# Kernel optimization log

Hardware: AMD Instinct MI355X
Metric: run time of the kernel (lower is better)

The kernel has to match this reference:

```python
import jax, jax.numpy as jnp
import numpy as np

N_M, N_D, E = 20000, 8000, 200000
F_IN, H, O = 384, 512, 256  # feature dim, hidden_channels, out_channels
H1 = O * 2                  # conv1 output channels = 512


def setup_inputs() -> dict:
    key = jax.random.key(0)
    ks = jax.random.split(key, 32)

    def w(k, shape):
        return jax.random.normal(k, shape, dtype=jnp.float32) * 0.02

    inp = {
        # node features
        "mirna_feat": jax.random.normal(ks[0], (N_M, F_IN), dtype=jnp.float32),
        "dis_feat": jax.random.normal(ks[1], (N_D, F_IN), dtype=jnp.float32),
        # node ids and edge list (miRNA -> disease); reverse edges are the flip
        "mirna_node_id": jnp.arange(N_M, dtype=jnp.int32),
        "dis_node_id": jnp.arange(N_D, dtype=jnp.int32),
        "edge_src": jax.random.randint(ks[2], (E,), 0, N_M, dtype=jnp.int32),
        "edge_dst": jax.random.randint(ks[3], (E,), 0, N_D, dtype=jnp.int32),
        # input projections + embeddings
        "Wm": w(ks[4], (F_IN, H)), "bm": jnp.zeros((H,), jnp.float32),
        "Wd": w(ks[5], (F_IN, H)), "bd": jnp.zeros((H,), jnp.float32),
        "mirna_emb": w(ks[6], (N_M, H)),
        "dis_emb": w(ks[7], (N_D, H)),
        # layer1 SAGEConv per edge type (md: miRNA->disease, dm: reverse)
        "W1_md_l": w(ks[8], (H, H1)), "b1_md": jnp.zeros((H1,), jnp.float32), "W1_md_r": w(ks[9], (H, H1)),
        "W1_dm_l": w(ks[10], (H, H1)), "b1_dm": jnp.zeros((H1,), jnp.float32), "W1_dm_r": w(ks[11], (H, H1)),
        # layer2 SAGEConv per edge type
        "W2_md_l": w(ks[12], (H1, O)), "b2_md": jnp.zeros((O,), jnp.float32), "W2_md_r": w(ks[13], (H1, O)),
        "W2_dm_l": w(ks[14], (H1, O)), "b2_dm": jnp.zeros((O,), jnp.float32), "W2_dm_r": w(ks[15], (H1, O)),
    }
    return inp


def _mean_agg(x_src, src_idx, dst_idx, n_dst):
    # gather src features per edge, segment-mean onto destinations (0 for isolated nodes)
    msg = jnp.take(x_src, src_idx, axis=0)               # [E, d]
    agg = jax.ops.segment_sum(msg, dst_idx, num_segments=n_dst)
    cnt = jax.ops.segment_sum(jnp.ones((dst_idx.shape[0],), x_src.dtype), dst_idx, num_segments=n_dst)
    return agg / jnp.maximum(cnt, 1.0)[:, None]


def _sage(x_src, x_dst, src_idx, dst_idx, Wl, bl, Wr):
    mean = _mean_agg(x_src, src_idx, dst_idx, x_dst.shape[0])
    return mean @ Wl + bl + x_dst @ Wr


def reference(mirna_feat, dis_feat, mirna_node_id, dis_node_id, edge_src, edge_dst,
              Wm, bm, Wd, bd, mirna_emb, dis_emb,
              W1_md_l, b1_md, W1_md_r, W1_dm_l, b1_dm, W1_dm_r,
              W2_md_l, b2_md, W2_md_r, W2_dm_l, b2_dm, W2_dm_r):
    # input encoders
    x_m = mirna_feat @ Wm + bm + jnp.take(mirna_emb, mirna_node_id, axis=0)
    x_d = dis_feat @ Wd + bd + jnp.take(dis_emb, dis_node_id, axis=0)
    # hetero SAGE layer 1 (each dst type has exactly one incoming edge type)
    h_d = _sage(x_m, x_d, edge_src, edge_dst, W1_md_l, b1_md, W1_md_r)
    h_m = _sage(x_d, x_m, edge_dst, edge_src, W1_dm_l, b1_dm, W1_dm_r)
    h_m, h_d = jax.nn.relu(h_m), jax.nn.relu(h_d)
    # hetero SAGE layer 2
    o_d = _sage(h_m, h_d, edge_src, edge_dst, W2_md_l, b2_md, W2_md_r)
    o_m = _sage(h_d, h_m, edge_dst, edge_src, W2_dm_l, b2_dm, W2_dm_r)
    return (o_m, o_d)
```

## Files before the change

### kernel.cpp

```cpp
#include <hip/hip_runtime.h>

#define DEVI __device__ __forceinline__

typedef __attribute__((ext_vector_type(8))) short bf16x8;
typedef __attribute__((ext_vector_type(4))) float f32x4;

static constexpr int NM = 20000, ND = 8000, NE = 200000;
static constexpr int FIN = 384, H = 512, H1 = 512, O = 256;

DEVI float bf2f(unsigned int u){ union{unsigned int i; float f;}v; v.i=u<<16; return v.f; }
DEVI unsigned int f2bf(float f){ union{float f; unsigned int i;}v; v.f=f;
  return (v.i + 0x7FFFu + ((v.i>>16)&1u))>>16; }

DEVI void gload16(const void* g, void* l){
  __builtin_amdgcn_global_load_lds((const __attribute__((address_space(1))) unsigned int*)g,
                                   (__attribute__((address_space(3))) unsigned int*)l, 16, 0, 0);
}

struct GPart {
  const unsigned short* A0;
  const unsigned short* A1;
  const unsigned short* WT;
  const float* bias;
  const float* emb;
  const int* ids;
  void* out;
  int M;
  int nbx;
};

template<int EPI>
__global__ __launch_bounds__(512, 8)
void gemm8w(GPart P0, GPart P1, int KA, int Ktot, int N)
{
  __shared__ unsigned short sA[2][128*32];
  __shared__ unsigned short sB[2][128*32];

  int bx = blockIdx.x;
  const bool snd = (bx >= P0.nbx);
  if (snd) bx -= P0.nbx;
  const unsigned short* A0  = snd ? P1.A0  : P0.A0;
  const unsigned short* A1  = snd ? P1.A1  : P0.A1;
  const unsigned short* WT  = snd ? P1.WT  : P0.WT;
  const float* bias         = snd ? P1.bias: P0.bias;
  const float* emb          = snd ? P1.emb : P0.emb;
  const int*   ids          = snd ? P1.ids : P0.ids;
  void*        outp         = snd ? P1.out : P0.out;
  const int    M            = snd ? P1.M   : P0.M;

  const int tid  = threadIdx.x;
  const int lane = tid & 63;
  const int wv   = tid >> 6;
  const int wr   = wv >> 1;
  const int wc   = wv & 1;
  const int bm0  = bx * 128;
  const int bn0  = blockIdx.y * 128;

  f32x4 acc[2][4];
  #pragma unroll
  for (int m=0;m<2;++m)
    #pragma unroll
    for (int n=0;n<4;++n) acc[m][n] = (f32x4){0.f,0.f,0.f,0.f};

  const int r = tid >> 2;
  const int c = tid & 3;
  const int KT = Ktot >> 5;

  auto STAGE = [&](int buf, int kt){
    const int kbase = kt << 5;
    const unsigned short* Ap; int ka, astr;
    if (kbase < KA) { Ap = A0; ka = kbase;      astr = KA; }
    else            { Ap = A1; ka = kbase - KA; astr = Ktot - KA; }
    int grA = bm0 + r; grA = grA < M ? grA : M-1;
    const int cc = (c ^ ((r>>1) & 3)) * 8;
    gload16(Ap + (size_t)grA*astr       + ka    + cc, &sA[buf][r*32 + c*8]);
    gload16(WT + (size_t)(bn0+r)*Ktot   + kbase + cc, &sB[buf][r*32 + c*8]);
  };

  STAGE(0, 0);
  __syncthreads();
  int cur = 0;
  for (int kt = 0; kt < KT; ++kt) {
    if (kt + 1 < KT) STAGE(cur ^ 1, kt + 1);
    bf16x8 af[2], bfr[4];
    #pragma unroll
    for (int m=0;m<2;++m){
      const int rl = wr*32 + m*16 + (lane&15);
      const int ch = (lane>>4) ^ ((rl>>1) & 3);
      af[m] = *(const bf16x8*)&sA[cur][rl*32 + ch*8];
    }
    #pragma unroll
    for (int n=0;n<4;++n){
      const int rl = wc*64 + n*16 + (lane&15);
      const int ch = (lane>>4) ^ ((rl>>1) & 3);
      bfr[n] = *(const bf16x8*)&sB[cur][rl*32 + ch*8];
    }
    #pragma unroll
    for (int m=0;m<2;++m)
      #pragma unroll
      for (int n=0;n<4;++n)
        acc[m][n] = __builtin_amdgcn_mfma_f32_16x16x32_bf16(af[m], bfr[n], acc[m][n], 0,0,0);
    __syncthreads();
    cur ^= 1;
  }

  const int cl = lane & 15;
  const int rg = lane >> 4;
  #pragma unroll
  for (int n=0;n<4;++n){
    const int col = bn0 + wc*64 + n*16 + cl;
    const float bv = bias[col];
    #pragma unroll
    for (int m=0;m<2;++m){
      const int rowb = bm0 + wr*32 + m*16 + rg*4;
      #pragma unroll
      for (int j=0;j<4;++j){
        const int row = rowb + j;
        if (row < M) {
          float v = acc[m][n][j] + bv;
          if constexpr (EPI==0) v += emb[(size_t)ids[row]*N + col];
          if constexpr (EPI==1) v = v > 0.f ? v : 0.f;
          if constexpr (EPI==2) ((float*)outp)[(size_t)row*N + col] = v;
          else ((unsigned short*)outp)[(size_t)row*N + col] = (unsigned short)f2bf(v);
        }
      }
    }
  }
}

__global__ __launch_bounds__(256)
void agg2(const unsigned short* __restrict__ Xm, const unsigned short* __restrict__ Xd,
          const int* __restrict__ offm, const int* __restrict__ ebs,
          const int* __restrict__ offd, const int* __restrict__ ebd,
          unsigned short* __restrict__ aggm, unsigned short* __restrict__ aggd)
{
  int node = blockIdx.x*4 + (threadIdx.x>>6);
  const unsigned short* X; const int* off; const int* nbr; unsigned short* out;
  if (node < NM){ X = Xd; off = offm; nbr = ebs; out = aggm; }
  else          { node -= NM; X = Xm; off = offd; nbr = ebd; out = aggd; }
  const int lane = threadIdx.x & 63;
  const int s = off[node], e = off[node+1];
  float a[8] = {0.f,0.f,0.f,0.f,0.f,0.f,0.f,0.f};
  for (int j = s; j < e; ++j){
    const int src = nbr[j];
    const uint4 v = *(const uint4*)(X + (size_t)src*H + lane*8);
    a[0]+=bf2f(v.x&0xffffu); a[1]+=bf2f(v.x>>16);
    a[2]+=bf2f(v.y&0xffffu); a[3]+=bf2f(v.y>>16);
    a[4]+=bf2f(v.z&0xffffu); a[5]+=bf2f(v.z>>16);
    a[6]+=bf2f(v.w&0xffffu); a[7]+=bf2f(v.w>>16);
  }
  const float inv = (e > s) ? 1.0f/(float)(e - s) : 0.0f;
  uint4 o;
  o.x = f2bf(a[0]*inv) | (f2bf(a[1]*inv)<<16);
  o.y = f2bf(a[2]*inv) | (f2bf(a[3]*inv)<<16);
  o.z = f2bf(a[4]*inv) | (f2bf(a[5]*inv)<<16);
  o.w = f2bf(a[6]*inv) | (f2bf(a[7]*inv)<<16);
  *(uint4*)(out + (size_t)node*H + lane*8) = o;
}

DEVI void tpart(int t, const float* __restrict__ in, unsigned short* __restrict__ out,
                int K, int N, int koff, int Kt)
{
  const int n = t / K, k = t - n*K;
  out[(size_t)n*Kt + koff + k] = (unsigned short)f2bf(in[(size_t)k*N + n]);
}

static constexpr int PREPW_BLOCKS = 7680;
static constexpr int CVT_BLOCKS   = 10500;
static constexpr int HIST_BLOCKS  = (NE + 255)/256;

__global__ __launch_bounds__(256)
void prep_all(const float* Wm, const float* Wd,
              const float* W1mdl, const float* W1mdr, const float* W1dml, const float* W1dmr,
              const float* W2mdl, const float* W2mdr, const float* W2dml, const float* W2dmr,
              unsigned short* WmT, unsigned short* WdT,
              unsigned short* W1mdT, unsigned short* W1dmT,
              unsigned short* W2mdT, unsigned short* W2dmT,
              const float* fm, const float* fd, unsigned short* om, unsigned short* od,
              const int* esrc, const int* edst, int* degm, int* degd)
{
  const int b = blockIdx.x;
  if (b < PREPW_BLOCKS) {
    int t = b*256 + threadIdx.x;
    const int sE = FIN*H, s1 = H*H1, s2 = H1*O;
    if (t < sE){ tpart(t, Wm,    WmT,   FIN, H, 0,   FIN ); return; } t -= sE;
    if (t < sE){ tpart(t, Wd,    WdT,   FIN, H, 0,   FIN ); return; } t -= sE;
    if (t < s1){ tpart(t, W1mdl, W1mdT, H,  H1, 0,   1024); return; } t -= s1;
    if (t < s1){ tpart(t, W1mdr, W1mdT, H,  H1, 512, 1024); return; } t -= s1;
    if (t < s1){ tpart(t, W1dml, W1dmT, H,  H1, 0,   1024); return; } t -= s1;
    if (t < s1){ tpart(t, W1dmr, W1dmT, H,  H1, 512, 1024); return; } t -= s1;
    if (t < s2){ tpart(t, W2mdl, W2mdT, H1, O,  0,   1024); return; } t -= s2;
    if (t < s2){ tpart(t, W2mdr, W2mdT, H1, O,  512, 1024); return; } t -= s2;
    if (t < s2){ tpart(t, W2dml, W2dmT, H1, O,  0,   1024); return; } t -= s2;
    if (t < s2){ tpart(t, W2dmr, W2dmT, H1, O,  512, 1024); return; }
  } else if (b < PREPW_BLOCKS + CVT_BLOCKS) {
    const long nm = (long)NM*FIN/4, nd = (long)ND*FIN/4;
    const long i = (long)(b - PREPW_BLOCKS)*256 + threadIdx.x;
    if (i >= nm+nd) return;
    const float4 v = (i < nm) ? ((const float4*)fm)[i] : ((const float4*)fd)[i-nm];
    uint2 o; o.x = f2bf(v.x) | (f2bf(v.y)<<16); o.y = f2bf(v.z) | (f2bf(v.w)<<16);
    if (i < nm) ((uint2*)om)[i] = o; else ((uint2*)od)[i-nm] = o;
  } else {
    const int e = (b - PREPW_BLOCKS - CVT_BLOCKS)*256 + threadIdx.x;
    if (e < NE){ atomicAdd(&degd[edst[e]], 1); atomicAdd(&degm[esrc[e]], 1); }
  }
}

__global__ __launch_bounds__(256)
void scan_k(const int* __restrict__ degd, int* __restrict__ offd, int* __restrict__ curd,
            const int* __restrict__ degm, int* __restrict__ offm, int* __restrict__ curm)
{
  const int* deg; int* off; int* cur; int n;
  if (blockIdx.x == 0){ deg=degd; off=offd; cur=curd; n=ND; }
  else                { deg=degm; off=offm; cur=curm; n=NM; }
  __shared__ int ps[257];
  const int t = threadIdx.x;
  const int chunk = (n + 255) >> 8;
  int lo = t*chunk;     if (lo > n) lo = n;
  int hi = lo + chunk;  if (hi > n) hi = n;
  int s = 0;
  for (int i=lo;i<hi;++i) s += deg[i];
  ps[t+1] = s;
  if (t==0) ps[0] = 0;
  __syncthreads();
  if (t==0){ for (int i=1;i<=256;++i) ps[i] += ps[i-1]; }
  __syncthreads();
  int run = ps[t];
  for (int i=lo;i<hi;++i){ off[i]=run; cur[i]=run; run += deg[i]; }
  if (t==0) off[n] = ps[256];
}

__global__ __launch_bounds__(256)
void fill_k(const int* __restrict__ esrc, const int* __restrict__ edst,
            int* __restrict__ curd, int* __restrict__ curm,
            int* __restrict__ ebd, int* __restrict__ ebs)
{
  const int e = blockIdx.x*256 + threadIdx.x;
  if (e < NE){
    const int s = esrc[e], d = edst[e];
    ebd[atomicAdd(&curd[d],1)] = s;
    ebs[atomicAdd(&curm[s],1)] = d;
  }
}

extern "C" void kernel_launch(void* const* d_in, const int* in_sizes, int n_in,
                              void* d_out, int out_size, void* d_ws, size_t ws_size,
                              hipStream_t stream)
{
  (void)in_sizes; (void)n_in; (void)out_size; (void)ws_size;
  const float* mirna_feat=(const float*)d_in[0];
  const float* dis_feat  =(const float*)d_in[1];
  const int*   m_id =(const int*)d_in[2];
  const int*   d_id =(const int*)d_in[3];
  const int*   esrc =(const int*)d_in[4];
  const int*   edst =(const int*)d_in[5];
  const float* Wm=(const float*)d_in[6];  const float* bm=(const float*)d_in[7];
  const float* Wd=(const float*)d_in[8];  const float* bd=(const float*)d_in[9];
  const float* m_emb=(const float*)d_in[10]; const float* d_emb=(const float*)d_in[11];
  const float* W1mdl=(const float*)d_in[12]; const float* b1md=(const float*)d_in[13];
  const float* W1mdr=(const float*)d_in[14];
  const float* W1dml=(const float*)d_in[15]; const float* b1dm=(const float*)d_in[16];
  const float* W1dmr=(const float*)d_in[17];
  const float* W2mdl=(const float*)d_in[18]; const float* b2md=(const float*)d_in[19];
  const float* W2mdr=(const float*)d_in[20];
  const float* W2dml=(const float*)d_in[21]; const float* b2dm=(const float*)d_in[22];
  const float* W2dmr=(const float*)d_in[23];

  size_t off = 0;
  char* base = (char*)d_ws;
  auto alloc = [&](size_t bytes)->void*{
    off = (off + 255) & ~(size_t)255;
    void* p = base + off; off += bytes; return p;
  };
  unsigned short* featm = (unsigned short*)alloc((size_t)NM*FIN*2);
  unsigned short* featd = (unsigned short*)alloc((size_t)ND*FIN*2);
  unsigned short* WmT   = (unsigned short*)alloc((size_t)H*FIN*2);
  unsigned short* WdT   = (unsigned short*)alloc((size_t)H*FIN*2);
  unsigned short* W1mdT = (unsigned short*)alloc((size_t)H1*1024*2);
  unsigned short* W1dmT = (unsigned short*)alloc((size_t)H1*1024*2);
  unsigned short* W2mdT = (unsigned short*)alloc((size_t)O*1024*2);
  unsigned short* W2dmT = (unsigned short*)alloc((size_t)O*1024*2);
  unsigned short* xm    = (unsigned short*)alloc((size_t)NM*H*2);
  unsigned short* xd    = (unsigned short*)alloc((size_t)ND*H*2);
  unsigned short* aggm  = (unsigned short*)alloc((size_t)NM*H*2);
  unsigned short* aggd  = (unsigned short*)alloc((size_t)ND*H*2);
  unsigned short* hm    = (unsigned short*)alloc((size_t)NM*H1*2);
  unsigned short* hd    = (unsigned short*)alloc((size_t)ND*H1*2);
  int* degd = (int*)alloc((size_t)(ND+NM)*4);
  int* degm = degd + ND;
  int* offd = (int*)alloc((size_t)(ND+1)*4);
  int* offm = (int*)alloc((size_t)(NM+1)*4);
  int* curd = (int*)alloc((size_t)ND*4);
  int* curm = (int*)alloc((size_t)NM*4);
  int* ebd  = (int*)alloc((size_t)NE*4);
  int* ebs  = (int*)alloc((size_t)NE*4);

  hipMemsetAsync(degd, 0, (size_t)(ND+NM)*4, stream);
  prep_all<<<PREPW_BLOCKS + CVT_BLOCKS + HIST_BLOCKS, 256, 0, stream>>>(
      Wm,Wd,W1mdl,W1mdr,W1dml,W1dmr,W2mdl,W2mdr,W2dml,W2dmr,
      WmT,WdT,W1mdT,W1dmT,W2mdT,W2dmT,
      mirna_feat, dis_feat, featm, featd,
      esrc, edst, degm, degd);
  scan_k<<<2,256,0,stream>>>(degd, offd, curd, degm, offm, curm);
  fill_k<<<(NE+255)/256,256,0,stream>>>(esrc, edst, curd, curm, ebd, ebs);

  {
    GPart p0{featm, featm, WmT, bm, m_emb, m_id, xm, NM, 157};
    GPart p1{featd, featd, WdT, bd, d_emb, d_id, xd, ND, 63};
    gemm8w<0><<<dim3(220,4),512,0,stream>>>(p0, p1, FIN, FIN, H);
  }
  agg2<<<(NM+ND)/4,256,0,stream>>>(xm, xd, offm, ebs, offd, ebd, aggm, aggd);
  {
    GPart p0{aggm, xm, W1dmT, b1dm, nullptr, nullptr, hm, NM, 157};
    GPart p1{aggd, xd, W1mdT, b1md, nullptr, nullptr, hd, ND, 63};
    gemm8w<1><<<dim3(220,4),512,0,stream>>>(p0, p1, H, 1024, H1);
  }
  agg2<<<(NM+ND)/4,256,0,stream>>>(hm, hd, offm, ebs, offd, ebd, aggm, aggd);
  float* out_m = (float*)d_out;
  float* out_d = out_m + (size_t)NM*O;
  {
    GPart p0{aggm, hm, W2dmT, b2dm, nullptr, nullptr, out_m, NM, 157};
    GPart p1{aggd, hd, W2mdT, b2md, nullptr, nullptr, out_d, ND, 63};
    gemm8w<2><<<dim3(220,2),512,0,stream>>>(p0, p1, H1, 1024, O);
  }
}
```

Before: 527.5 us.

## Triple-buffer GEMM LDS pipeline and pre-convert embeddings to bf16

The GEMM kernel moves from double to triple buffering of LDS tiles. It prefetches three k-steps ahead, waits with explicit vmcnt/lgkmcnt counters and raw barriers, and lowers the occupancy hint to 6 waves, all to hide global-load latency better. Separately, the embedding tables are converted to bf16 in the prep kernel, written into the hm/hd buffers before those are used, so the encoder epilogue reads half the bytes. The cost is an extra conversion pass over the embeddings and more LDS per block. The clamped redundant prefetch on the last tiles also adds some extra loads.

```diff
diff --git a/kernel.cpp b/kernel.cpp
--- a/kernel.cpp
+++ b/kernel.cpp
@@ -22,7 +22,7 @@
   const unsigned short* A1;
   const unsigned short* WT;
   const float* bias;
-  const float* emb;
+  const unsigned short* emb;
   const int* ids;
   void* out;
   int M;
@@ -30,11 +30,11 @@
 };
 
 template<int EPI>
-__global__ __launch_bounds__(512, 8)
+__global__ __launch_bounds__(512, 6)
 void gemm8w(GPart P0, GPart P1, int KA, int Ktot, int N)
 {
-  __shared__ unsigned short sA[2][128*32];
-  __shared__ unsigned short sB[2][128*32];
+  __shared__ unsigned short sA[3][128*32];
+  __shared__ unsigned short sB[3][128*32];
 
   int bx = blockIdx.x;
   const bool snd = (bx >= P0.nbx);
@@ -43,7 +43,7 @@
   const unsigned short* A1  = snd ? P1.A1  : P0.A1;
   const unsigned short* WT  = snd ? P1.WT  : P0.WT;
   const float* bias         = snd ? P1.bias: P0.bias;
-  const float* emb          = snd ? P1.emb : P0.emb;
+  const unsigned short* emb = snd ? P1.emb : P0.emb;
   const int*   ids          = snd ? P1.ids : P0.ids;
   void*        outp         = snd ? P1.out : P0.out;
   const int    M            = snd ? P1.M   : P0.M;
@@ -77,11 +77,11 @@
     gload16(WT + (size_t)(bn0+r)*Ktot   + kbase + cc, &sB[buf][r*32 + c*8]);
   };
 
-  STAGE(0, 0);
-  __syncthreads();
+  STAGE(0, 0); STAGE(1, 1); STAGE(2, 2);
   int cur = 0;
   for (int kt = 0; kt < KT; ++kt) {
-    if (kt + 1 < KT) STAGE(cur ^ 1, kt + 1);
+    asm volatile("s_waitcnt vmcnt(4)" ::: "memory");
+    __builtin_amdgcn_s_barrier();
     bf16x8 af[2], bfr[4];
     #pragma unroll
     for (int m=0;m<2;++m){
@@ -100,8 +100,12 @@
       #pragma unroll
       for (int n=0;n<4;++n)
         acc[m][n] = __builtin_amdgcn_mfma_f32_16x16x32_bf16(af[m], bfr[n], acc[m][n], 0,0,0);
-    __syncthreads();
-    cur ^= 1;
+    asm volatile("s_waitcnt lgkmcnt(0)" ::: "memory");
+    __builtin_amdgcn_sched_barrier(0);
+    __builtin_amdgcn_s_barrier();
+    const int nxt = (kt+3 < KT) ? (kt+3) : (KT-1);
+    STAGE(cur, nxt);
+    cur = (cur==2) ? 0 : cur+1;
   }
 
   const int cl = lane & 15;
@@ -118,7 +122,7 @@
         const int row = rowb + j;
         if (row < M) {
           float v = acc[m][n][j] + bv;
-          if constexpr (EPI==0) v += emb[(size_t)ids[row]*N + col];
+          if constexpr (EPI==0) v += bf2f(emb[(size_t)ids[row]*N + col]);
           if constexpr (EPI==1) v = v > 0.f ? v : 0.f;
           if constexpr (EPI==2) ((float*)outp)[(size_t)row*N + col] = v;
           else ((unsigned short*)outp)[(size_t)row*N + col] = (unsigned short)f2bf(v);
@@ -167,6 +171,7 @@
 
 static constexpr int PREPW_BLOCKS = 7680;
 static constexpr int CVT_BLOCKS   = 10500;
+static constexpr int EMB_BLOCKS   = 14000;
 static constexpr int HIST_BLOCKS  = (NE + 255)/256;
 
 __global__ __launch_bounds__(256)
@@ -177,6 +182,7 @@
               unsigned short* W1mdT, unsigned short* W1dmT,
               unsigned short* W2mdT, unsigned short* W2dmT,
               const float* fm, const float* fd, unsigned short* om, unsigned short* od,
+              const float* memb, const float* demb, unsigned short* embm, unsigned short* embd,
               const int* esrc, const int* edst, int* degm, int* degd)
 {
   const int b = blockIdx.x;
@@ -200,8 +206,15 @@
     const float4 v = (i < nm) ? ((const float4*)fm)[i] : ((const float4*)fd)[i-nm];
     uint2 o; o.x = f2bf(v.x) | (f2bf(v.y)<<16); o.y = f2bf(v.z) | (f2bf(v.w)<<16);
     if (i < nm) ((uint2*)om)[i] = o; else ((uint2*)od)[i-nm] = o;
+  } else if (b < PREPW_BLOCKS + CVT_BLOCKS + EMB_BLOCKS) {
+    const long nm = (long)NM*H/4, nd = (long)ND*H/4;
+    const long i = (long)(b - PREPW_BLOCKS - CVT_BLOCKS)*256 + threadIdx.x;
+    if (i >= nm+nd) return;
+    const float4 v = (i < nm) ? ((const float4*)memb)[i] : ((const float4*)demb)[i-nm];
+    uint2 o; o.x = f2bf(v.x) | (f2bf(v.y)<<16); o.y = f2bf(v.z) | (f2bf(v.w)<<16);
+    if (i < nm) ((uint2*)embm)[i] = o; else ((uint2*)embd)[i-nm] = o;
   } else {
-    const int e = (b - PREPW_BLOCKS - CVT_BLOCKS)*256 + threadIdx.x;
+    const int e = (b - PREPW_BLOCKS - CVT_BLOCKS - EMB_BLOCKS)*256 + threadIdx.x;
     if (e < NE){ atomicAdd(&degd[edst[e]], 1); atomicAdd(&degm[esrc[e]], 1); }
   }
 }
@@ -295,18 +308,22 @@
   int* ebd  = (int*)alloc((size_t)NE*4);
   int* ebs  = (int*)alloc((size_t)NE*4);
 
+  unsigned short* embm = hm;
+  unsigned short* embd = hd;
+
   hipMemsetAsync(degd, 0, (size_t)(ND+NM)*4, stream);
-  prep_all<<<PREPW_BLOCKS + CVT_BLOCKS + HIST_BLOCKS, 256, 0, stream>>>(
+  prep_all<<<PREPW_BLOCKS + CVT_BLOCKS + EMB_BLOCKS + HIST_BLOCKS, 256, 0, stream>>>(
       Wm,Wd,W1mdl,W1mdr,W1dml,W1dmr,W2mdl,W2mdr,W2dml,W2dmr,
       WmT,WdT,W1mdT,W1dmT,W2mdT,W2dmT,
       mirna_feat, dis_feat, featm, featd,
+      m_emb, d_emb, embm, embd,
       esrc, edst, degm, degd);
   scan_k<<<2,256,0,stream>>>(degd, offd, curd, degm, offm, curm);
   fill_k<<<(NE+255)/256,256,0,stream>>>(esrc, edst, curd, curm, ebd, ebs);
 
   {
-    GPart p0{featm, featm, WmT, bm, m_emb, m_id, xm, NM, 157};
-    GPart p1{featd, featd, WdT, bd, d_emb, d_id, xd, ND, 63};
+    GPart p0{featm, featm, WmT, bm, embm, m_id, xm, NM, 157};
+    GPart p1{featd, featd, WdT, bd, embd, d_id, xd, ND, 63};
     gemm8w<0><<<dim3(220,4),512,0,stream>>>(p0, p1, FIN, FIN, H);
   }
   agg2<<<(NM+ND)/4,256,0,stream>>>(xm, xd, offm, ebs, offd, ebd, aggm, aggd);
```

Result: slower. 541.3 us (+2.6%).
